# Optimization experiments

Measured on AMD Instinct MI355X. Metric: run time of the kernel, lower is better.

The kernel has to match this reference:

```python
import jax, jax.numpy as jnp
import numpy as np

B, H, L, D = 2, 16, 2048, 64


def setup_inputs() -> dict:
    key = jax.random.key(0)
    kq, kk, kv = jax.random.split(key, 3)
    return {
        "query": jax.random.normal(kq, (B, H, L, D), dtype=jnp.float32),
        "key": jax.random.normal(kk, (B, H, L, D), dtype=jnp.float32),
        "value": jax.random.normal(kv, (B, H, L, D), dtype=jnp.float32),
        "dhead": D,
        "causal": 1,
    }


def reference(query, key, value, dhead, causal):
    # mode='dhead': muP attention with scale 1/dhead (not 1/sqrt(dhead)).
    # Inputs/outputs in [B, H, L, D] layout (the torch code transposes to
    # [B, L, H, D] for the einsum and transposes back; net layout is the same).
    scale = 1.0 / dhead
    a = jnp.einsum('bhld,bhLd->bhlL', query, key) * scale  # [B,H,L,L]
    if causal:
        seq = a.shape[-1]
        mask = jnp.tril(jnp.ones((seq, seq), dtype=bool))  # [L,L]
        a = jnp.where(mask, a, jnp.float32(-jnp.inf))
    a = jax.nn.softmax(a, axis=-1)
    out = jnp.einsum('bhlL,bhLd->bhld', a, value)  # [B,H,L,D]
    return out
```

## Files before the change

kernel.cpp:

```cpp
#include <hip/hip_runtime.h>

#define BHH 32
#define SEQ 2048
#define DH 64
#define BQ 64
#define BK 64
#define NKT (SEQ / BK)
#define NQB (SEQ / BQ)
#define NT  (BHH * NKT)

typedef __attribute__((ext_vector_type(8))) _Float16 half8_t;
typedef __attribute__((ext_vector_type(4))) _Float16 half4_t;
typedef __attribute__((ext_vector_type(2))) _Float16 half2_t;
typedef __attribute__((ext_vector_type(4))) float f32x4;

__device__ __forceinline__ void async_copy16(const void* g, const void* lds) {
    __builtin_amdgcn_global_load_lds(
        (const __attribute__((address_space(1))) unsigned int*)g,
        (__attribute__((address_space(3))) unsigned int*)lds, 16, 0, 0);
}

__device__ __forceinline__ half2_t pkrtz(float a, float b) {
    return __builtin_bit_cast(half2_t, __builtin_amdgcn_cvt_pkrtz(a, b));
}

__global__ __launch_bounds__(256) void prep_kv(const float* __restrict__ K,
                                               const float* __restrict__ V,
                                               _Float16* __restrict__ Kf,
                                               _Float16* __restrict__ Vf) {
    __shared__ _Float16 l[64 * 76];
    const int t = threadIdx.x;
    const int wave = t >> 6, lane = t & 63, ln15 = lane & 15, quad = lane >> 4;
    const int row = t >> 2, col0 = (t & 3) * 16;
    int b = blockIdx.x;

    if (b < NT) {
        const float4* src = (const float4*)(K + (size_t)b * 4096 + row * 64 + col0);
        #pragma unroll
        for (int q = 0; q < 2; ++q) {
            float4 f0 = src[q * 2], f1 = src[q * 2 + 1];
            half8_t w = { (_Float16)f0.x, (_Float16)f0.y, (_Float16)f0.z, (_Float16)f0.w,
                          (_Float16)f1.x, (_Float16)f1.y, (_Float16)f1.z, (_Float16)f1.w };
            *(half8_t*)&l[row * 72 + col0 + q * 8] = w;
        }
        __syncthreads();
        #pragma unroll
        for (int p = 0; p < 2; ++p) {
            const int bid = wave * 2 + p, c = bid >> 1, k0 = bid & 1;
            half8_t w = *(const half8_t*)&l[(c * 16 + ln15) * 72 + k0 * 32 + quad * 8];
            *(half8_t*)&Kf[(size_t)b * 4096 + bid * 512 + lane * 8] = w;
        }
    } else {
        b -= NT;
        const float4* src = (const float4*)(V + (size_t)b * 4096 + row * 64 + col0);
        #pragma unroll
        for (int q = 0; q < 4; ++q) {
            float4 f = src[q];
            half4_t w = { (_Float16)f.x, (_Float16)f.y, (_Float16)f.z, (_Float16)f.w };
            *(half4_t*)&l[row * 76 + col0 + q * 4] = w;
        }
        __syncthreads();
        #pragma unroll
        for (int p = 0; p < 2; ++p) {
            const int f = wave * 2 + p, cn = f >> 1, k1 = f & 1;
            half8_t w;
            #pragma unroll
            for (int jj = 0; jj < 8; ++jj) {
                const int krow = k1 * 32 + ((jj & 4) << 2) + quad * 4 + (jj & 3);
                w[jj] = l[krow * 76 + cn * 16 + ln15];
            }
            *(half8_t*)&Vf[(size_t)b * 4096 + f * 512 + lane * 8] = w;
        }
    }
}

__global__ __launch_bounds__(256, 4) void fattn_kernel(
        const float* __restrict__ Q, const _Float16* __restrict__ Kf,
        const _Float16* __restrict__ Vf, float* __restrict__ O) {
    const int bh = blockIdx.x & 31;
    const int r = blockIdx.x >> 5, j = r & 7, rnd = r >> 3;
    const int qb = (rnd == 0) ? 31 - j : (rnd == 1) ? 16 + j
                 : (rnd == 2) ? 15 - j : j;
    const int tid  = threadIdx.x;
    const int wave = tid >> 6;
    const int lane = tid & 63;
    const int ln15 = lane & 15;
    const int quad = lane >> 4;

    __shared__ _Float16 ldsK[2][4096];
    __shared__ _Float16 ldsV[2][4096];

    const size_t base = (size_t)bh * SEQ * DH;
    const int q0   = qb * BQ;
    const int qrow = q0 + wave * 16;
    const size_t tb = (size_t)(bh * NKT) * 4096;

    const _Float16* gsrc = ((wave < 2) ? Kf : Vf) + tb + (wave & 1) * 2048 + lane * 8;
    _Float16* dstA = ((wave < 2) ? &ldsK[0][0] : &ldsV[0][0]) + (wave & 1) * 2048;
    _Float16* dstB = ((wave < 2) ? &ldsK[1][0] : &ldsV[1][0]) + (wave & 1) * 2048;

    #define STAGE(kt_, d_) do {                                          \
        const _Float16* s_ = gsrc + (size_t)(kt_) * 4096;                \
        _Float16* dd_ = (d_);                                            \
        _Pragma("unroll")                                                \
        for (int i_ = 0; i_ < 4; ++i_)                                   \
            async_copy16(s_ + i_ * 512, dd_ + i_ * 512);                 \
    } while (0)

    STAGE(0, dstA);

    const float qscale = 1.44269504f / 64.0f;
    half8_t qfrag[2];
    {
        const float* qp = Q + base + (size_t)(qrow + ln15) * DH + quad * 8;
        #pragma unroll
        for (int k0 = 0; k0 < 2; ++k0) {
            float4 a = *(const float4*)(qp + k0 * 32);
            float4 b2 = *(const float4*)(qp + k0 * 32 + 4);
            qfrag[k0] = (half8_t){
                (_Float16)(a.x * qscale), (_Float16)(a.y * qscale),
                (_Float16)(a.z * qscale), (_Float16)(a.w * qscale),
                (_Float16)(b2.x * qscale), (_Float16)(b2.y * qscale),
                (_Float16)(b2.z * qscale), (_Float16)(b2.w * qscale) };
        }
    }

    f32x4 acc[4] = {};
    float l_lane = 0.f;

    const _Float16* kA = &ldsK[0][0] + lane * 8;
    const _Float16* kB = &ldsK[1][0] + lane * 8;
    const _Float16* vA = &ldsV[0][0] + lane * 8;
    const _Float16* vB = &ldsV[1][0] + lane * 8;
    const int myrel = wave * 16 + ln15;
    const int kq4 = quad * 4;

    __syncthreads();

    for (int kt = 0; kt <= qb; ++kt) {
        const _Float16* kk = (kt & 1) ? kB : kA;
        const _Float16* vv = (kt & 1) ? vB : vA;
        if (kt < qb) STAGE(kt + 1, ((kt + 1) & 1) ? dstB : dstA);

        f32x4 st[4];
        #pragma unroll
        for (int c = 0; c < 4; ++c) {
            half8_t kf0 = *(const half8_t*)(kk + c * 1024);
            half8_t kf1 = *(const half8_t*)(kk + c * 1024 + 512);
            f32x4 a = {};
            a = __builtin_amdgcn_mfma_f32_16x16x32_f16(kf0, qfrag[0], a, 0, 0, 0);
            a = __builtin_amdgcn_mfma_f32_16x16x32_f16(kf1, qfrag[1], a, 0, 0, 0);
            st[c] = a;
        }

        float p[4][4];
        #pragma unroll
        for (int c = 0; c < 4; ++c)
            #pragma unroll
            for (int rr = 0; rr < 4; ++rr)
                p[c][rr] = __builtin_amdgcn_exp2f(st[c][rr]);

        if (kt == qb) {
            #pragma unroll
            for (int c = 0; c < 4; ++c)
                #pragma unroll
                for (int rr = 0; rr < 4; ++rr)
                    if (c * 16 + kq4 + rr > myrel) p[c][rr] = 0.f;
        }

        float s0 = (p[0][0] + p[0][1]) + (p[0][2] + p[0][3]);
        float s1 = (p[1][0] + p[1][1]) + (p[1][2] + p[1][3]);
        float s2 = (p[2][0] + p[2][1]) + (p[2][2] + p[2][3]);
        float s3 = (p[3][0] + p[3][1]) + (p[3][2] + p[3][3]);
        l_lane += (s0 + s1) + (s2 + s3);

        union P8 { half2_t h2[4]; half8_t h8; };
        P8 u0, u1;
        u0.h2[0] = pkrtz(p[0][0], p[0][1]);
        u0.h2[1] = pkrtz(p[0][2], p[0][3]);
        u0.h2[2] = pkrtz(p[1][0], p[1][1]);
        u0.h2[3] = pkrtz(p[1][2], p[1][3]);
        u1.h2[0] = pkrtz(p[2][0], p[2][1]);
        u1.h2[1] = pkrtz(p[2][2], p[2][3]);
        u1.h2[2] = pkrtz(p[3][0], p[3][1]);
        u1.h2[3] = pkrtz(p[3][2], p[3][3]);
        half8_t pb0 = u0.h8, pb1 = u1.h8;

        #pragma unroll
        for (int cn = 0; cn < 4; ++cn) {
            half8_t vf0 = *(const half8_t*)(vv + cn * 1024);
            acc[cn] = __builtin_amdgcn_mfma_f32_16x16x32_f16(vf0, pb0, acc[cn], 0, 0, 0);
            half8_t vf1 = *(const half8_t*)(vv + cn * 1024 + 512);
            acc[cn] = __builtin_amdgcn_mfma_f32_16x16x32_f16(vf1, pb1, acc[cn], 0, 0, 0);
        }
        __syncthreads();
    }

    {
        float l_i = l_lane + __shfl_xor(l_lane, 16);
        l_i += __shfl_xor(l_i, 32);
        const float rl = 1.0f / l_i;
        float* op = O + base + (size_t)(qrow + ln15) * DH;
        #pragma unroll
        for (int cn = 0; cn < 4; ++cn) {
            float4 o;
            o.x = acc[cn][0] * rl;
            o.y = acc[cn][1] * rl;
            o.z = acc[cn][2] * rl;
            o.w = acc[cn][3] * rl;
            *(float4*)(op + cn * 16 + kq4) = o;
        }
    }
    #undef STAGE
}

extern "C" void kernel_launch(void* const* d_in, const int* in_sizes, int n_in,
                              void* d_out, int out_size, void* d_ws, size_t ws_size,
                              hipStream_t stream) {
    const float* Q = (const float*)d_in[0];
    const float* K = (const float*)d_in[1];
    const float* V = (const float*)d_in[2];
    float* O = (float*)d_out;
    _Float16* Kf = (_Float16*)d_ws;
    _Float16* Vf = Kf + (size_t)NT * 4096;
    prep_kv<<<2 * NT, 256, 0, stream>>>(K, V, Kf, Vf);
    fattn_kernel<<<NQB * BHH, 256, 0, stream>>>(Q, Kf, Vf, O);
}
```

Measured before the change: 121.9 us.

## Triple-buffer K/V tiles with prefetch depth two and manual waitcnt barriers

Moves K/V LDS staging from double to triple buffering so the tile two iterations ahead is prefetched. Each loop iteration now opens with a single hand-written s_waitcnt vmcnt(4) plus barrier in place of the closing __syncthreads, so only the oldest tile's copies must land before compute. It also raises wave priority around the PV MFMA block. LDS grows to 48KB per block, which forces the launch bound down from 4 to 3 blocks per CU and risks lower occupancy. Correctness rests on the inline-asm vmcnt count matching exactly four outstanding async copies per tile.

```diff
diff --git a/kernel.cpp b/kernel.cpp
--- a/kernel.cpp
+++ b/kernel.cpp
@@ -74,7 +74,7 @@
     }
 }
 
-__global__ __launch_bounds__(256, 4) void fattn_kernel(
+__global__ __launch_bounds__(256, 3) void fattn_kernel(
         const float* __restrict__ Q, const _Float16* __restrict__ Kf,
         const _Float16* __restrict__ Vf, float* __restrict__ O) {
     const int bh = blockIdx.x & 31;
@@ -87,8 +87,8 @@
     const int ln15 = lane & 15;
     const int quad = lane >> 4;
 
-    __shared__ _Float16 ldsK[2][4096];
-    __shared__ _Float16 ldsV[2][4096];
+    __shared__ _Float16 ldsK[3][4096];
+    __shared__ _Float16 ldsV[3][4096];
 
     const size_t base = (size_t)bh * SEQ * DH;
     const int q0   = qb * BQ;
@@ -96,18 +96,16 @@
     const size_t tb = (size_t)(bh * NKT) * 4096;
 
     const _Float16* gsrc = ((wave < 2) ? Kf : Vf) + tb + (wave & 1) * 2048 + lane * 8;
-    _Float16* dstA = ((wave < 2) ? &ldsK[0][0] : &ldsV[0][0]) + (wave & 1) * 2048;
-    _Float16* dstB = ((wave < 2) ? &ldsK[1][0] : &ldsV[1][0]) + (wave & 1) * 2048;
-
-    #define STAGE(kt_, d_) do {                                          \
+    _Float16* sdst0 = ((wave < 2) ? &ldsK[0][0] : &ldsV[0][0]) + (wave & 1) * 2048;
+
+    #define STAGE(kt_, dd_) do {                                         \
         const _Float16* s_ = gsrc + (size_t)(kt_) * 4096;                \
-        _Float16* dd_ = (d_);                                            \
-        _Pragma("unroll")                                                \
-        for (int i_ = 0; i_ < 4; ++i_)                                   \
-            async_copy16(s_ + i_ * 512, dd_ + i_ * 512);                 \
+        _Float16* d_ = (dd_);                                            \
+        async_copy16(s_,        d_);                                     \
+        async_copy16(s_ + 512,  d_ + 512);                               \
+        async_copy16(s_ + 1024, d_ + 1024);                              \
+        async_copy16(s_ + 1536, d_ + 1536);                              \
     } while (0)
-
-    STAGE(0, dstA);
 
     const float qscale = 1.44269504f / 64.0f;
     half8_t qfrag[2];
@@ -124,23 +122,30 @@
                 (_Float16)(b2.z * qscale), (_Float16)(b2.w * qscale) };
         }
     }
+    asm volatile("" ::: "memory");
+
+    STAGE(0, sdst0);
+    STAGE(1, sdst0 + 4096);
 
     f32x4 acc[4] = {};
     float l_lane = 0.f;
 
-    const _Float16* kA = &ldsK[0][0] + lane * 8;
-    const _Float16* kB = &ldsK[1][0] + lane * 8;
-    const _Float16* vA = &ldsV[0][0] + lane * 8;
-    const _Float16* vB = &ldsV[1][0] + lane * 8;
+    const _Float16* kbase = &ldsK[0][0] + lane * 8;
+    const _Float16* vbase = &ldsV[0][0] + lane * 8;
     const int myrel = wave * 16 + ln15;
     const int kq4 = quad * 4;
 
-    __syncthreads();
-
+    int bs = 0, b2 = 2;
     for (int kt = 0; kt <= qb; ++kt) {
-        const _Float16* kk = (kt & 1) ? kB : kA;
-        const _Float16* vv = (kt & 1) ? vB : vA;
-        if (kt < qb) STAGE(kt + 1, ((kt + 1) & 1) ? dstB : dstA);
+        if (kt < qb)
+            asm volatile("s_waitcnt vmcnt(4) lgkmcnt(0)\n\ts_barrier" ::: "memory");
+        else
+            asm volatile("s_waitcnt vmcnt(0) lgkmcnt(0)\n\ts_barrier" ::: "memory");
+
+        if (kt + 2 <= qb) STAGE(kt + 2, sdst0 + b2 * 4096);
+
+        const _Float16* kk = kbase + bs * 4096;
+        const _Float16* vv = vbase + bs * 4096;
 
         f32x4 st[4];
         #pragma unroll
@@ -186,6 +191,7 @@
         u1.h2[3] = pkrtz(p[3][2], p[3][3]);
         half8_t pb0 = u0.h8, pb1 = u1.h8;
 
+        __builtin_amdgcn_s_setprio(1);
         #pragma unroll
         for (int cn = 0; cn < 4; ++cn) {
             half8_t vf0 = *(const half8_t*)(vv + cn * 1024);
@@ -193,7 +199,10 @@
             half8_t vf1 = *(const half8_t*)(vv + cn * 1024 + 512);
             acc[cn] = __builtin_amdgcn_mfma_f32_16x16x32_f16(vf1, pb1, acc[cn], 0, 0, 0);
         }
-        __syncthreads();
+        __builtin_amdgcn_s_setprio(0);
+
+        bs = (bs == 2) ? 0 : bs + 1;
+        b2 = (b2 == 2) ? 0 : b2 + 1;
     }
 
     {
```

Measured after the change: 122.6 us. No clear change (+0.5%).

## Shrink attention blocks to 2 waves and pair light/heavy query tiles per block

Applied to the files above, without the earlier changes.

The attention kernel now uses 128-thread blocks, each covering 32 query rows, and every block runs two passes over complementary query tiles (pr and 63-pr). This balances causal work evenly across blocks instead of relying on a block-index reordering. Each wave now stages a full K or V tile (8 async copies) and uses raw waitcnt/barrier asm. The trade-off is that K/V tiles are re-read per 32-row tile, which doubles LDS staging traffic per query row, and occupancy is lower.

```diff
diff --git a/kernel.cpp b/kernel.cpp
--- a/kernel.cpp
+++ b/kernel.cpp
@@ -3,10 +3,8 @@
 #define BHH 32
 #define SEQ 2048
 #define DH 64
-#define BQ 64
 #define BK 64
 #define NKT (SEQ / BK)
-#define NQB (SEQ / BQ)
 #define NT  (BHH * NKT)
 
 typedef __attribute__((ext_vector_type(8))) _Float16 half8_t;
@@ -74,13 +72,11 @@
     }
 }
 
-__global__ __launch_bounds__(256, 4) void fattn_kernel(
+__global__ __launch_bounds__(128, 2) void fattn_kernel(
         const float* __restrict__ Q, const _Float16* __restrict__ Kf,
         const _Float16* __restrict__ Vf, float* __restrict__ O) {
     const int bh = blockIdx.x & 31;
-    const int r = blockIdx.x >> 5, j = r & 7, rnd = r >> 3;
-    const int qb = (rnd == 0) ? 31 - j : (rnd == 1) ? 16 + j
-                 : (rnd == 2) ? 15 - j : j;
+    const int pr = blockIdx.x >> 5;
     const int tid  = threadIdx.x;
     const int wave = tid >> 6;
     const int lane = tid & 63;
@@ -91,124 +87,132 @@
     __shared__ _Float16 ldsV[2][4096];
 
     const size_t base = (size_t)bh * SEQ * DH;
-    const int q0   = qb * BQ;
-    const int qrow = q0 + wave * 16;
     const size_t tb = (size_t)(bh * NKT) * 4096;
 
-    const _Float16* gsrc = ((wave < 2) ? Kf : Vf) + tb + (wave & 1) * 2048 + lane * 8;
-    _Float16* dstA = ((wave < 2) ? &ldsK[0][0] : &ldsV[0][0]) + (wave & 1) * 2048;
-    _Float16* dstB = ((wave < 2) ? &ldsK[1][0] : &ldsV[1][0]) + (wave & 1) * 2048;
-
-    #define STAGE(kt_, d_) do {                                          \
+    const _Float16* gsrc = (wave ? Vf : Kf) + tb + lane * 8;
+    _Float16* dst0 = (wave ? &ldsV[0][0] : &ldsK[0][0]);
+    _Float16* dst1 = (wave ? &ldsV[1][0] : &ldsK[1][0]);
+
+    #define STAGE(kt_, dd_) do {                                         \
         const _Float16* s_ = gsrc + (size_t)(kt_) * 4096;                \
-        _Float16* dd_ = (d_);                                            \
+        _Float16* d_ = (dd_);                                            \
         _Pragma("unroll")                                                \
-        for (int i_ = 0; i_ < 4; ++i_)                                   \
-            async_copy16(s_ + i_ * 512, dd_ + i_ * 512);                 \
+        for (int f_ = 0; f_ < 8; ++f_)                                   \
+            async_copy16(s_ + f_ * 512, d_ + f_ * 512);                  \
     } while (0)
 
-    STAGE(0, dstA);
-
+    const _Float16* kbase = &ldsK[0][0] + lane * 8;
+    const _Float16* vbase = &ldsV[0][0] + lane * 8;
+    const int kq4 = quad * 4;
     const float qscale = 1.44269504f / 64.0f;
-    half8_t qfrag[2];
-    {
-        const float* qp = Q + base + (size_t)(qrow + ln15) * DH + quad * 8;
-        #pragma unroll
-        for (int k0 = 0; k0 < 2; ++k0) {
-            float4 a = *(const float4*)(qp + k0 * 32);
-            float4 b2 = *(const float4*)(qp + k0 * 32 + 4);
-            qfrag[k0] = (half8_t){
-                (_Float16)(a.x * qscale), (_Float16)(a.y * qscale),
-                (_Float16)(a.z * qscale), (_Float16)(a.w * qscale),
-                (_Float16)(b2.x * qscale), (_Float16)(b2.y * qscale),
-                (_Float16)(b2.z * qscale), (_Float16)(b2.w * qscale) };
-        }
-    }
-
-    f32x4 acc[4] = {};
-    float l_lane = 0.f;
-
-    const _Float16* kA = &ldsK[0][0] + lane * 8;
-    const _Float16* kB = &ldsK[1][0] + lane * 8;
-    const _Float16* vA = &ldsV[0][0] + lane * 8;
-    const _Float16* vB = &ldsV[1][0] + lane * 8;
-    const int myrel = wave * 16 + ln15;
-    const int kq4 = quad * 4;
-
-    __syncthreads();
-
-    for (int kt = 0; kt <= qb; ++kt) {
-        const _Float16* kk = (kt & 1) ? kB : kA;
-        const _Float16* vv = (kt & 1) ? vB : vA;
-        if (kt < qb) STAGE(kt + 1, ((kt + 1) & 1) ? dstB : dstA);
-
-        f32x4 st[4];
-        #pragma unroll
-        for (int c = 0; c < 4; ++c) {
-            half8_t kf0 = *(const half8_t*)(kk + c * 1024);
-            half8_t kf1 = *(const half8_t*)(kk + c * 1024 + 512);
-            f32x4 a = {};
-            a = __builtin_amdgcn_mfma_f32_16x16x32_f16(kf0, qfrag[0], a, 0, 0, 0);
-            a = __builtin_amdgcn_mfma_f32_16x16x32_f16(kf1, qfrag[1], a, 0, 0, 0);
-            st[c] = a;
-        }
-
-        float p[4][4];
-        #pragma unroll
-        for (int c = 0; c < 4; ++c)
-            #pragma unroll
-            for (int rr = 0; rr < 4; ++rr)
-                p[c][rr] = __builtin_amdgcn_exp2f(st[c][rr]);
-
-        if (kt == qb) {
+
+    union P8 { half2_t h2[4]; half8_t h8; };
+
+    #pragma unroll 1
+    for (int pass = 0; pass < 2; ++pass) {
+        const int q32  = pass ? (63 - pr) : pr;
+        const int qb64 = q32 >> 1;
+        const int nkt  = qb64 + 1;
+        const int qrow = q32 * 32 + wave * 16;
+        const int relrow = (q32 & 1) * 32 + wave * 16 + ln15;
+
+        if (pass)
+            asm volatile("s_barrier" ::: "memory");
+
+        STAGE(0, dst0);
+
+        half8_t qfrag[2];
+        {
+            const float* qp = Q + base + (size_t)(qrow + ln15) * DH + quad * 8;
+            #pragma unroll
+            for (int k0 = 0; k0 < 2; ++k0) {
+                float4 a = *(const float4*)(qp + k0 * 32);
+                float4 b2 = *(const float4*)(qp + k0 * 32 + 4);
+                qfrag[k0] = (half8_t){
+                    (_Float16)(a.x * qscale), (_Float16)(a.y * qscale),
+                    (_Float16)(a.z * qscale), (_Float16)(a.w * qscale),
+                    (_Float16)(b2.x * qscale), (_Float16)(b2.y * qscale),
+                    (_Float16)(b2.z * qscale), (_Float16)(b2.w * qscale) };
+            }
+        }
+        asm volatile("s_waitcnt vmcnt(0) lgkmcnt(0)\n\ts_barrier" ::: "memory");
+
+        f32x4 acc[4] = {};
+        float l_lane = 0.f;
+
+        for (int kt = 0; kt < nkt; ++kt) {
+            const _Float16* kk = kbase + (kt & 1) * 4096;
+            const _Float16* vv = vbase + (kt & 1) * 4096;
+            if (kt + 1 < nkt) STAGE(kt + 1, (kt & 1) ? dst0 : dst1);
+
+            f32x4 st[4];
+            #pragma unroll
+            for (int c = 0; c < 4; ++c) {
+                half8_t kf0 = *(const half8_t*)(kk + c * 1024);
+                half8_t kf1 = *(const half8_t*)(kk + c * 1024 + 512);
+                f32x4 a = {};
+                a = __builtin_amdgcn_mfma_f32_16x16x32_f16(kf0, qfrag[0], a, 0, 0, 0);
+                a = __builtin_amdgcn_mfma_f32_16x16x32_f16(kf1, qfrag[1], a, 0, 0, 0);
+                st[c] = a;
+            }
+
+            float p[4][4];
             #pragma unroll
             for (int c = 0; c < 4; ++c)
                 #pragma unroll
                 for (int rr = 0; rr < 4; ++rr)
-                    if (c * 16 + kq4 + rr > myrel) p[c][rr] = 0.f;
-        }
-
-        float s0 = (p[0][0] + p[0][1]) + (p[0][2] + p[0][3]);
-        float s1 = (p[1][0] + p[1][1]) + (p[1][2] + p[1][3]);
-        float s2 = (p[2][0] + p[2][1]) + (p[2][2] + p[2][3]);
-        float s3 = (p[3][0] + p[3][1]) + (p[3][2] + p[3][3]);
-        l_lane += (s0 + s1) + (s2 + s3);
-
-        union P8 { half2_t h2[4]; half8_t h8; };
-        P8 u0, u1;
-        u0.h2[0] = pkrtz(p[0][0], p[0][1]);
-        u0.h2[1] = pkrtz(p[0][2], p[0][3]);
-        u0.h2[2] = pkrtz(p[1][0], p[1][1]);
-        u0.h2[3] = pkrtz(p[1][2], p[1][3]);
-        u1.h2[0] = pkrtz(p[2][0], p[2][1]);
-        u1.h2[1] = pkrtz(p[2][2], p[2][3]);
-        u1.h2[2] = pkrtz(p[3][0], p[3][1]);
-        u1.h2[3] = pkrtz(p[3][2], p[3][3]);
-        half8_t pb0 = u0.h8, pb1 = u1.h8;
-
-        #pragma unroll
-        for (int cn = 0; cn < 4; ++cn) {
-            half8_t vf0 = *(const half8_t*)(vv + cn * 1024);
-            acc[cn] = __builtin_amdgcn_mfma_f32_16x16x32_f16(vf0, pb0, acc[cn], 0, 0, 0);
-            half8_t vf1 = *(const half8_t*)(vv + cn * 1024 + 512);
-            acc[cn] = __builtin_amdgcn_mfma_f32_16x16x32_f16(vf1, pb1, acc[cn], 0, 0, 0);
-        }
-        __syncthreads();
-    }
-
-    {
-        float l_i = l_lane + __shfl_xor(l_lane, 16);
-        l_i += __shfl_xor(l_i, 32);
-        const float rl = 1.0f / l_i;
-        float* op = O + base + (size_t)(qrow + ln15) * DH;
-        #pragma unroll
-        for (int cn = 0; cn < 4; ++cn) {
-            float4 o;
-            o.x = acc[cn][0] * rl;
-            o.y = acc[cn][1] * rl;
-            o.z = acc[cn][2] * rl;
-            o.w = acc[cn][3] * rl;
-            *(float4*)(op + cn * 16 + kq4) = o;
+                    p[c][rr] = __builtin_amdgcn_exp2f(st[c][rr]);
+
+            if (kt == qb64) {
+                #pragma unroll
+                for (int c = 0; c < 4; ++c)
+                    #pragma unroll
+                    for (int rr = 0; rr < 4; ++rr)
+                        if (c * 16 + kq4 + rr > relrow) p[c][rr] = 0.f;
+            }
+
+            float s0 = (p[0][0] + p[0][1]) + (p[0][2] + p[0][3]);
+            float s1 = (p[1][0] + p[1][1]) + (p[1][2] + p[1][3]);
+            float s2 = (p[2][0] + p[2][1]) + (p[2][2] + p[2][3]);
+            float s3 = (p[3][0] + p[3][1]) + (p[3][2] + p[3][3]);
+            l_lane += (s0 + s1) + (s2 + s3);
+
+            P8 u0, u1;
+            u0.h2[0] = pkrtz(p[0][0], p[0][1]);
+            u0.h2[1] = pkrtz(p[0][2], p[0][3]);
+            u0.h2[2] = pkrtz(p[1][0], p[1][1]);
+            u0.h2[3] = pkrtz(p[1][2], p[1][3]);
+            u1.h2[0] = pkrtz(p[2][0], p[2][1]);
+            u1.h2[1] = pkrtz(p[2][2], p[2][3]);
+            u1.h2[2] = pkrtz(p[3][0], p[3][1]);
+            u1.h2[3] = pkrtz(p[3][2], p[3][3]);
+            half8_t pb0 = u0.h8, pb1 = u1.h8;
+
+            #pragma unroll
+            for (int cn = 0; cn < 4; ++cn) {
+                half8_t vf0 = *(const half8_t*)(vv + cn * 1024);
+                acc[cn] = __builtin_amdgcn_mfma_f32_16x16x32_f16(vf0, pb0, acc[cn], 0, 0, 0);
+                half8_t vf1 = *(const half8_t*)(vv + cn * 1024 + 512);
+                acc[cn] = __builtin_amdgcn_mfma_f32_16x16x32_f16(vf1, pb1, acc[cn], 0, 0, 0);
+            }
+
+            asm volatile("s_waitcnt vmcnt(0) lgkmcnt(0)\n\ts_barrier" ::: "memory");
+        }
+
+        {
+            float l_i = l_lane + __shfl_xor(l_lane, 16);
+            l_i += __shfl_xor(l_i, 32);
+            const float rl = 1.0f / l_i;
+            float* op = O + base + (size_t)(qrow + ln15) * DH;
+            #pragma unroll
+            for (int cn = 0; cn < 4; ++cn) {
+                float4 o;
+                o.x = acc[cn][0] * rl;
+                o.y = acc[cn][1] * rl;
+                o.z = acc[cn][2] * rl;
+                o.w = acc[cn][3] * rl;
+                *(float4*)(op + cn * 16 + kq4) = o;
+            }
         }
     }
     #undef STAGE
@@ -224,5 +228,5 @@
     _Float16* Kf = (_Float16*)d_ws;
     _Float16* Vf = Kf + (size_t)NT * 4096;
     prep_kv<<<2 * NT, 256, 0, stream>>>(K, V, Kf, Vf);
-    fattn_kernel<<<NQB * BHH, 256, 0, stream>>>(Q, Kf, Vf, O);
-}
+    fattn_kernel<<<1024, 128, 0, stream>>>(Q, Kf, Vf, O);
+}
```

New measurement: 126.6 us. +3.8%, slower.
